# Performance work log

Measured on AMD Instinct MI355X. Metric: run time of the kernel, lower is better.

The kernel has to match this reference:

```python
import jax, jax.numpy as jnp
import numpy as np

N = 50000      # num_nodes
E = 800000     # num_edges (avg degree 16)
D = 128        # input_dim = hidden_dim = output_dim
L = 3          # num_layers
EPS = 1e-5     # BatchNorm eps


def setup_inputs() -> dict:
    key = jax.random.key(0)
    k_x, k_e, k_w, k_b = jax.random.split(key, 4)
    x = jax.random.normal(k_x, (N, D), dtype=jnp.float32)
    edge_index = jax.random.randint(k_e, (2, E), 0, N, dtype=jnp.int32)
    # Stacked per-layer params: GCN weight/bias + BatchNorm gamma/beta
    Ws = jax.random.normal(k_w, (L, D, D), dtype=jnp.float32) * (1.0 / np.sqrt(D))
    bs = jax.random.normal(k_b, (L, D), dtype=jnp.float32) * 0.01
    gammas = jnp.ones((L, D), dtype=jnp.float32)
    betas = jnp.zeros((L, D), dtype=jnp.float32)
    return {"x": x, "edge_index": edge_index, "Ws": Ws, "bs": bs,
            "gammas": gammas, "betas": betas}


def reference(x, edge_index, Ws, bs, gammas, betas):
    """CausalGNN forward: L x (GCNConv -> BN(train stats) -> ReLU[not last]) with residuals.
    Dropout p=0 (deterministic). GCNConv is PyG-style: add self-loops, symmetric
    D^{-1/2} (A+I) D^{-1/2} normalization, linear transform + bias."""
    src, dst = edge_index[0], edge_index[1]
    # degree including self-loop (+1), computed at aggregation index
    deg = jax.ops.segment_sum(jnp.ones((E,), jnp.float32), dst, num_segments=N) + 1.0
    dis = jax.lax.rsqrt(deg)                       # deg >= 1, safe
    norm = dis[src] * dis[dst]                      # [E] edge norm
    self_norm = dis * dis                           # [N] self-loop norm = 1/deg

    for i in range(L):
        h = x @ Ws[i]                               # [N, D]
        # scatter-add aggregation of normalized neighbor messages
        agg = jax.ops.segment_sum(h[src] * norm[:, None], dst, num_segments=N)
        agg = agg + self_norm[:, None] * h + bs[i]
        # BatchNorm1d (training mode: biased batch statistics over nodes)
        mean = jnp.mean(agg, axis=0)
        var = jnp.mean(jnp.square(agg - mean), axis=0)
        y = gammas[i] * (agg - mean) * jax.lax.rsqrt(var + EPS) + betas[i]
        if i < L - 1:
            y = jax.nn.relu(y)
        x = x + y if i > 0 else y                   # residual (dims match)
    return x
```

## Files before the change

kernel.cpp:

```cpp
#include <hip/hip_runtime.h>
#include <hip/hip_bf16.h>
#include <hip/hip_fp16.h>

#define N_ 50000
#define E_ 800000
#define D_ 128
#define L_ 3

#define GG 782
#define NB 391
#define BCAP 3072
#define PB 200
#define PE 4000

typedef _Float16 half8 __attribute__((ext_vector_type(8)));
typedef float f32x4 __attribute__((ext_vector_type(4)));


__device__ inline float4 hcvt(uint2 u) {
    __half2 h0 = *(__half2*)&u.x;
    __half2 h1 = *(__half2*)&u.y;
    float2 f0 = __half22float2(h0);
    float2 f1 = __half22float2(h1);
    return make_float4(f0.x, f0.y, f1.x, f1.y);
}

__device__ inline unsigned pkh(float a, float b) {
    __half2 h = __floats2half2_rn(a, b);
    return *(unsigned*)&h;
}

__device__ inline unsigned short pkh1(float a) {
    _Float16 h = (_Float16)a;
    return *(unsigned short*)&h;
}


__global__ __launch_bounds__(256) void k_part(const int* __restrict__ src,
                                              const int* __restrict__ dst,
                                              const float* __restrict__ Ws,
                                              unsigned short* __restrict__ Wb,
                                              int* __restrict__ bucket_cnt,
                                              unsigned int* __restrict__ binned) {
    int b = blockIdx.x;
    if (b >= PB) {
        int l = b - PB;
        const float* Wl = Ws + l * 16384;
        unsigned short* Wo = Wb + l * 16384;
        for (int i = threadIdx.x; i < 16384; i += 256) {
            int n = i >> 7, k = i & 127;
            Wo[n * 128 + k] = pkh1(Wl[k * 128 + n]);
        }
        return;
    }
    __shared__ int hcnt[NB];
    __shared__ int hbase[NB];
    int t = threadIdx.x;
    for (int i = t; i < NB; i += 256) hcnt[i] = 0;
    __syncthreads();
    int e0 = b * PE;
    int dreg[16], sreg[16], oreg[16];
#pragma unroll
    for (int it = 0; it < 16; ++it) {
        int i = t + it * 256;
        if (i < PE) {
            int e = e0 + i;
            int d = dst[e];
            dreg[it] = d;
            sreg[it] = src[e];
            oreg[it] = atomicAdd(&hcnt[d >> 7], 1);
        }
    }
    __syncthreads();
    for (int i = t; i < NB; i += 256) {
        int c = hcnt[i];
        hbase[i] = c ? atomicAdd(&bucket_cnt[i], c) : 0;
    }
    __syncthreads();
#pragma unroll
    for (int it = 0; it < 16; ++it) {
        int i = t + it * 256;
        if (i < PE) {
            int d = dreg[it];
            int bk = d >> 7;
            binned[bk * BCAP + hbase[bk] + oreg[it]] =
                ((unsigned)(d & 127) << 16) | (unsigned)sreg[it];
        }
    }
}


__global__ __launch_bounds__(512) void k_bscan(const int* __restrict__ bucket_cnt,
                                               int* __restrict__ bucket_base,
                                               int* __restrict__ row_ptr) {
    __shared__ int wsum[8];
    int t = threadIdx.x;
    int lane = t & 63, wid = t >> 6;
    int v = (t < NB) ? bucket_cnt[t] : 0;
    int inc = v;
#pragma unroll
    for (int o = 1; o < 64; o <<= 1) {
        int u = __shfl_up(inc, o);
        if (lane >= o) inc += u;
    }
    if (lane == 63) wsum[wid] = inc;
    __syncthreads();
    if (wid == 0) {
        int w = (lane < 8) ? wsum[lane] : 0;
#pragma unroll
        for (int o = 1; o < 8; o <<= 1) {
            int u = __shfl_up(w, o);
            if (lane >= o) w += u;
        }
        if (lane < 8) wsum[lane] = w;
    }
    __syncthreads();
    int woff = wid ? wsum[wid - 1] : 0;
    if (t < NB) bucket_base[t] = inc + woff - v;
    if (t == 0) row_ptr[N_] = E_;
}


__device__ __forceinline__ void bin_body(const unsigned int* __restrict__ binned,
                                         const int* __restrict__ bucket_cnt,
                                         const int* __restrict__ bucket_base,
                                         int* __restrict__ row_ptr,
                                         float* __restrict__ dis,
                                         int* __restrict__ csr_src, int b) {
    __shared__ int h[128];
    __shared__ int hs[128];
    __shared__ int wtot[2];
    int t = threadIdx.x;
    if (t < 128) h[t] = 0;
    __syncthreads();
    int cnt  = bucket_cnt[b];
    int base = bucket_base[b];
    const unsigned int* bp = binned + b * BCAP;
    unsigned int pk[12];
    int off[12];
#pragma unroll
    for (int it = 0; it < 12; ++it) {
        int i = t + it * 256;
        if (i < cnt) {
            unsigned int p = bp[i];
            pk[it] = p;
            off[it] = atomicAdd(&h[p >> 16], 1);
        }
    }
    __syncthreads();
    int v = (t < 128) ? h[t] : 0;
    int lane = t & 63, wid = t >> 6;
    int inc = v;
#pragma unroll
    for (int o = 1; o < 64; o <<= 1) {
        int u = __shfl_up(inc, o);
        if (lane >= o) inc += u;
    }
    if (lane == 63 && wid < 2) wtot[wid] = inc;
    __syncthreads();
    if (wid == 1) inc += wtot[0];
    if (t < 128) {
        hs[t] = inc - v;
        int node = b * 128 + t;
        if (node < N_) {
            dis[node] = rsqrtf((float)v + 1.0f);
            row_ptr[node] = base + (inc - v);
        }
    }
    __syncthreads();
#pragma unroll
    for (int it = 0; it < 12; ++it) {
        int i = t + it * 256;
        if (i < cnt) {
            unsigned int p = pk[it];
            csr_src[base + hs[p >> 16] + off[it]] = (int)(p & 0xFFFFu);
        }
    }
}


__device__ __forceinline__ void gemm_body(const float* __restrict__ Xin,
                                          const unsigned short* __restrict__ Wb,
                                          uint4* __restrict__ Hb,
                                          const float* __restrict__ st,
                                          const float* __restrict__ gamma,
                                          const float* __restrict__ beta,
                                          const unsigned short* __restrict__ resH,
                                          unsigned short* __restrict__ xoutH,
                                          int blk) {
    __shared__ unsigned short wt[128 * 136];
    __shared__ unsigned short xb[64 * 136];
    __shared__ float sab[256];
    int t  = threadIdx.x;
    int r0 = blk * 64;

    if (st) {
        if (t < 128) {
            float s = 0.f, s2 = 0.f;
#pragma unroll
            for (int k = 0; k < 8; ++k) {
                s  += st[k * 256 + t];
                s2 += st[k * 256 + 128 + t];
            }
            float mean = s * (1.0f / N_);
            float var  = s2 * (1.0f / N_) - mean * mean;
            float a = gamma[t] * rsqrtf(var + 1e-5f);
            sab[t]       = a;
            sab[128 + t] = beta[t] - mean * a;
        }
        __syncthreads();
    }

#pragma unroll
    for (int j = 0; j < 8; ++j) {
        int i = t + 256 * j;
        int row = i >> 4, c16 = i & 15;
        *(uint4*)&wt[row * 136 + c16 * 8] = ((const uint4*)Wb)[i];
    }
#pragma unroll
    for (int j = 0; j < 8; ++j) {
        int g   = t + 256 * j;
        int row = g >> 5;
        int c4  = (g & 31) * 4;
        int gr  = r0 + row;
        float4 v = make_float4(0.f, 0.f, 0.f, 0.f);
        if (gr < N_) {
            v = *(const float4*)(Xin + gr * 128 + c4);
            if (st) {
                v.x = fmaxf(sab[c4] * v.x + sab[128 + c4], 0.f);
                v.y = fmaxf(sab[c4 + 1] * v.y + sab[128 + c4 + 1], 0.f);
                v.z = fmaxf(sab[c4 + 2] * v.z + sab[128 + c4 + 2], 0.f);
                v.w = fmaxf(sab[c4 + 3] * v.w + sab[128 + c4 + 3], 0.f);
                if (resH) {
                    float4 rr = hcvt(*(const uint2*)(resH + gr * 128 + c4));
                    v.x += rr.x; v.y += rr.y; v.z += rr.z; v.w += rr.w;
                }
            }
        }
        uint2 p;
        p.x = pkh(v.x, v.y);
        p.y = pkh(v.z, v.w);
        if (st && gr < N_) *(uint2*)(xoutH + gr * 128 + c4) = p;
        *(uint2*)&xb[row * 136 + c4] = p;
    }
    __syncthreads();

    int wv   = t >> 6;
    int lane = t & 63;
    int ln   = lane & 15;
    int quad = lane >> 4;

    const unsigned short* arow = &xb[(wv * 16 + ln) * 136 + quad * 8];
    half8 af[4];
#pragma unroll
    for (int ks = 0; ks < 4; ++ks) af[ks] = *(const half8*)(arow + ks * 32);

    f32x4 acc[8];
#pragma unroll
    for (int ct = 0; ct < 8; ++ct) acc[ct] = (f32x4){0.f, 0.f, 0.f, 0.f};

#pragma unroll
    for (int ct = 0; ct < 8; ++ct) {
        const unsigned short* wp = &wt[(ct * 16 + ln) * 136 + quad * 8];
#pragma unroll
        for (int ks = 0; ks < 4; ++ks) {
            half8 bf = *(const half8*)(wp + ks * 32);
            acc[ct] = __builtin_amdgcn_mfma_f32_16x16x32_f16(af[ks], bf, acc[ct], 0, 0, 0);
        }
    }

    __syncthreads();
#pragma unroll
    for (int ct = 0; ct < 8; ++ct) {
#pragma unroll
        for (int reg = 0; reg < 4; ++reg) {
            int lrow = wv * 16 + quad * 4 + reg;
            xb[lrow * 136 + ct * 16 + ln] = pkh1(acc[ct][reg]);
        }
    }
    __syncthreads();
#pragma unroll
    for (int j = 0; j < 4; ++j) {
        int i = t + 256 * j;
        int row = i >> 4, c16 = i & 15;
        int gr = r0 + row;
        if (gr < N_) Hb[gr * 16 + c16] = *(uint4*)&xb[row * 136 + c16 * 8];
    }
}


__global__ __launch_bounds__(256) void k_fillg(const unsigned int* __restrict__ binned,
                                               const int* __restrict__ bucket_cnt,
                                               const int* __restrict__ bucket_base,
                                               int* __restrict__ row_ptr,
                                               float* __restrict__ dis,
                                               int* __restrict__ csr_src,
                                               const float* __restrict__ x,
                                               const unsigned short* __restrict__ Wb,
                                               uint4* __restrict__ Hb) {
    int b = blockIdx.x;
    if (b < NB) {
        bin_body(binned, bucket_cnt, bucket_base, row_ptr, dis, csr_src, b);
    } else {
        gemm_body(x, Wb, Hb, nullptr, nullptr, nullptr, nullptr, nullptr, b - NB);
    }
}


__global__ __launch_bounds__(256) void k_gemm(const float* __restrict__ Xin,
                                              const unsigned short* __restrict__ Wb,
                                              uint4* __restrict__ Hb,
                                              const float* __restrict__ st,
                                              const float* __restrict__ gamma,
                                              const float* __restrict__ beta,
                                              const unsigned short* __restrict__ resH,
                                              unsigned short* __restrict__ xoutH) {
    gemm_body(Xin, Wb, Hb, st, gamma, beta, resH, xoutH, blockIdx.x);
}


__global__ __launch_bounds__(256) void k_agg(const uint4* __restrict__ Hb,
                                             const int* __restrict__ row_ptr,
                                             const int* __restrict__ csr_src,
                                             const float* __restrict__ dis,
                                             const float* __restrict__ bias,
                                             float4* __restrict__ AGG,
                                             float* __restrict__ stats2) {
    int tid  = threadIdx.x;
    int sub  = tid >> 4;
    int lane = tid & 15;
    int node = blockIdx.x * 16 + sub;

    int beg = row_ptr[node], end = row_ptr[node + 1];
    float dn = dis[node];
    uint4 su = Hb[node * 16 + lane];
    float4 f0s = hcvt(make_uint2(su.x, su.y));
    float4 f1s = hcvt(make_uint2(su.z, su.w));
    float4 acc0, acc1;
    acc0.x = dn * f0s.x; acc0.y = dn * f0s.y; acc0.z = dn * f0s.z; acc0.w = dn * f0s.w;
    acc1.x = dn * f1s.x; acc1.y = dn * f1s.y; acc1.z = dn * f1s.z; acc1.w = dn * f1s.w;

    for (int c = beg; c < end; c += 16) {
        int m = end - c; if (m > 16) m = 16;
        int idx = 0; float dsv = 0.f;
        if (lane < m) { idx = csr_src[c + lane]; dsv = dis[idx]; }
        int j = 0;
        for (; j + 4 <= m; j += 4) {
            int s0 = __shfl(idx, j, 16);
            int s1 = __shfl(idx, j + 1, 16);
            int s2 = __shfl(idx, j + 2, 16);
            int s3 = __shfl(idx, j + 3, 16);
            float d0 = __shfl(dsv, j, 16);
            float d1 = __shfl(dsv, j + 1, 16);
            float d2 = __shfl(dsv, j + 2, 16);
            float d3 = __shfl(dsv, j + 3, 16);
            uint4 a0 = Hb[s0 * 16 + lane];
            uint4 a1 = Hb[s1 * 16 + lane];
            uint4 a2 = Hb[s2 * 16 + lane];
            uint4 a3 = Hb[s3 * 16 + lane];
            float4 f00 = hcvt(make_uint2(a0.x, a0.y)), f01 = hcvt(make_uint2(a0.z, a0.w));
            float4 f10 = hcvt(make_uint2(a1.x, a1.y)), f11 = hcvt(make_uint2(a1.z, a1.w));
            float4 f20 = hcvt(make_uint2(a2.x, a2.y)), f21 = hcvt(make_uint2(a2.z, a2.w));
            float4 f30 = hcvt(make_uint2(a3.x, a3.y)), f31 = hcvt(make_uint2(a3.z, a3.w));
            acc0.x += d0 * f00.x + d1 * f10.x + d2 * f20.x + d3 * f30.x;
            acc0.y += d0 * f00.y + d1 * f10.y + d2 * f20.y + d3 * f30.y;
            acc0.z += d0 * f00.z + d1 * f10.z + d2 * f20.z + d3 * f30.z;
            acc0.w += d0 * f00.w + d1 * f10.w + d2 * f20.w + d3 * f30.w;
            acc1.x += d0 * f01.x + d1 * f11.x + d2 * f21.x + d3 * f31.x;
            acc1.y += d0 * f01.y + d1 * f11.y + d2 * f21.y + d3 * f31.y;
            acc1.z += d0 * f01.z + d1 * f11.z + d2 * f21.z + d3 * f31.z;
            acc1.w += d0 * f01.w + d1 * f11.w + d2 * f21.w + d3 * f31.w;
        }
        for (; j < m; ++j) {
            int s0 = __shfl(idx, j, 16);
            float d0 = __shfl(dsv, j, 16);
            uint4 a0 = Hb[s0 * 16 + lane];
            float4 f00 = hcvt(make_uint2(a0.x, a0.y)), f01 = hcvt(make_uint2(a0.z, a0.w));
            acc0.x += d0 * f00.x; acc0.y += d0 * f00.y;
            acc0.z += d0 * f00.z; acc0.w += d0 * f00.w;
            acc1.x += d0 * f01.x; acc1.y += d0 * f01.y;
            acc1.z += d0 * f01.z; acc1.w += d0 * f01.w;
        }
    }

    float4 b0 = *(const float4*)(bias + lane * 8);
    float4 b1 = *(const float4*)(bias + lane * 8 + 4);
    float4 r0, r1;
    r0.x = dn * acc0.x + b0.x; r0.y = dn * acc0.y + b0.y;
    r0.z = dn * acc0.z + b0.z; r0.w = dn * acc0.w + b0.w;
    r1.x = dn * acc1.x + b1.x; r1.y = dn * acc1.y + b1.y;
    r1.z = dn * acc1.z + b1.z; r1.w = dn * acc1.w + b1.w;
    AGG[node * 32 + lane * 2]     = r0;
    AGG[node * 32 + lane * 2 + 1] = r1;

    __shared__ float sbuf[16][128];
    float4* sp = (float4*)&sbuf[sub][lane * 8];
    sp[0] = r0; sp[1] = r1;
    __syncthreads();
    if (tid < 128) {
        float s = 0.f, s2 = 0.f;
#pragma unroll
        for (int k = 0; k < 16; ++k) {
            float v = sbuf[k][tid];
            s += v; s2 += v * v;
        }
        float* stp = stats2 + (blockIdx.x & 7) * 256;
        atomicAdd(&stp[tid], s);
        atomicAdd(&stp[128 + tid], s2);
    }
}


__global__ __launch_bounds__(256) void k_normF(const float4* __restrict__ AGG,
                                               const unsigned short* __restrict__ resH,
                                               const float* __restrict__ st,
                                               const float* __restrict__ gamma,
                                               const float* __restrict__ beta,
                                               float4* __restrict__ OUT) {
    __shared__ float sab[256];
    int t = threadIdx.x;
    if (t < 128) {
        float s = 0.f, s2 = 0.f;
#pragma unroll
        for (int k = 0; k < 8; ++k) {
            s  += st[k * 256 + t];
            s2 += st[k * 256 + 128 + t];
        }
        float mean = s * (1.0f / N_);
        float var  = s2 * (1.0f / N_) - mean * mean;
        float a = gamma[t] * rsqrtf(var + 1e-5f);
        sab[t]       = a;
        sab[128 + t] = beta[t] - mean * a;
    }
    __syncthreads();
    for (int i = blockIdx.x * 256 + t; i < N_ * 32; i += gridDim.x * 256) {
        int f4 = (i & 31) * 4;
        float4 v = AGG[i];
        float4 rr = hcvt(((const uint2*)resH)[i]);
        v.x = sab[f4] * v.x + sab[128 + f4] + rr.x;
        v.y = sab[f4 + 1] * v.y + sab[128 + f4 + 1] + rr.y;
        v.z = sab[f4 + 2] * v.z + sab[128 + f4 + 2] + rr.z;
        v.w = sab[f4 + 3] * v.w + sab[128 + f4 + 3] + rr.w;
        OUT[i] = v;
    }
}


extern "C" void kernel_launch(void* const* d_in, const int* in_sizes, int n_in,
                              void* d_out, int out_size, void* d_ws, size_t ws_size,
                              hipStream_t stream) {
    const float* x      = (const float*)d_in[0];
    const int*   ei     = (const int*)d_in[1];
    const float* Ws     = (const float*)d_in[2];
    const float* bs     = (const float*)d_in[3];
    const float* gammas = (const float*)d_in[4];
    const float* betas  = (const float*)d_in[5];
    float* out = (float*)d_out;

    const int* src = ei;
    const int* dst = ei + E_;

    char* w = (char*)d_ws;
    float* stats2      = (float*)(w + 0);
    int*   bucket_cnt  = (int*)(w + 24576);
    int*   bucket_base = (int*)(w + 26144);
    int*   row_ptr     = (int*)(w + 27712);
    float* dis         = (float*)(w + 227728);
    int*   csr_src     = (int*)(w + 427728);
    uint4* Hb          = (uint4*)(w + 3627776);
    unsigned short* XBh = (unsigned short*)(w + 16427776);
    unsigned short* Wb  = (unsigned short*)(w + 29227776);
    float* AGG = out;

    unsigned int* binned = (unsigned int*)XBh;

    hipMemsetAsync(d_ws, 0, 26144, stream);

    k_part<<<PB + 3, 256, 0, stream>>>(src, dst, Ws, Wb, bucket_cnt, binned);
    k_bscan<<<1, 512, 0, stream>>>(bucket_cnt, bucket_base, row_ptr);
    k_fillg<<<NB + GG, 256, 0, stream>>>(binned, bucket_cnt, bucket_base, row_ptr,
                                         dis, csr_src, x, Wb, Hb);

    k_agg<<<N_ / 16, 256, 0, stream>>>(Hb, row_ptr, csr_src, dis, bs,
                                       (float4*)AGG, stats2);
    k_gemm<<<GG, 256, 0, stream>>>(AGG, Wb + 16384, Hb,
                                   stats2, gammas, betas, nullptr, XBh);
    k_agg<<<N_ / 16, 256, 0, stream>>>(Hb, row_ptr, csr_src, dis, bs + D_,
                                       (float4*)AGG, stats2 + 2048);
    k_gemm<<<GG, 256, 0, stream>>>(AGG, Wb + 32768, Hb,
                                   stats2 + 2048, gammas + D_, betas + D_, XBh, XBh);
    k_agg<<<N_ / 16, 256, 0, stream>>>(Hb, row_ptr, csr_src, dis, bs + 2 * D_,
                                       (float4*)AGG, stats2 + 4096);
    k_normF<<<1024, 256, 0, stream>>>((const float4*)AGG, XBh,
                                      stats2 + 4096, gammas + 2 * D_, betas + 2 * D_,
                                      (float4*)out);
}
```

Measured before the change: 263.4 us.

## Prescale GEMM output by dis, store intermediate aggregates in fp16, unroll gather by 8

The GEMM epilogue now multiplies each output row by its dis value, so layers 2 and 3 aggregation skip the per-edge dis lookup and multiply. The first two aggregation outputs are written as fp16 and read back as fp16 by the next GEMM, halving that intermediate traffic. The gather loop also gains an 8-wide unrolled stage to keep more loads in flight. The cost is extra fp16 rounding of the aggregate and of the prescaled features before batch-norm statistics, plus higher register pressure from the wider unroll.

```diff
diff --git a/kernel.cpp b/kernel.cpp
--- a/kernel.cpp
+++ b/kernel.cpp
@@ -179,8 +179,10 @@
 }
 
 
-__device__ __forceinline__ void gemm_body(const float* __restrict__ Xin,
+template <bool IN16>
+__device__ __forceinline__ void gemm_body(const void* __restrict__ Xin,
                                           const unsigned short* __restrict__ Wb,
+                                          const float* __restrict__ disp,
                                           uint4* __restrict__ Hb,
                                           const float* __restrict__ st,
                                           const float* __restrict__ gamma,
@@ -225,7 +227,11 @@
         int gr  = r0 + row;
         float4 v = make_float4(0.f, 0.f, 0.f, 0.f);
         if (gr < N_) {
-            v = *(const float4*)(Xin + gr * 128 + c4);
+            if constexpr (IN16) {
+                v = hcvt(*(const uint2*)((const unsigned short*)Xin + gr * 128 + c4));
+            } else {
+                v = *(const float4*)((const float*)Xin + gr * 128 + c4);
+            }
             if (st) {
                 v.x = fmaxf(sab[c4] * v.x + sab[128 + c4], 0.f);
                 v.y = fmaxf(sab[c4 + 1] * v.y + sab[128 + c4 + 1], 0.f);
@@ -269,13 +275,21 @@
         }
     }
 
+    float dr[4] = {1.f, 1.f, 1.f, 1.f};
+    if (disp) {
+#pragma unroll
+        for (int reg = 0; reg < 4; ++reg) {
+            int r = r0 + wv * 16 + quad * 4 + reg;
+            dr[reg] = disp[r < N_ ? r : (N_ - 1)];
+        }
+    }
     __syncthreads();
 #pragma unroll
     for (int ct = 0; ct < 8; ++ct) {
 #pragma unroll
         for (int reg = 0; reg < 4; ++reg) {
             int lrow = wv * 16 + quad * 4 + reg;
-            xb[lrow * 136 + ct * 16 + ln] = pkh1(acc[ct][reg]);
+            xb[lrow * 136 + ct * 16 + ln] = pkh1(acc[ct][reg] * dr[reg]);
         }
     }
     __syncthreads();
@@ -302,29 +316,32 @@
     if (b < NB) {
         bin_body(binned, bucket_cnt, bucket_base, row_ptr, dis, csr_src, b);
     } else {
-        gemm_body(x, Wb, Hb, nullptr, nullptr, nullptr, nullptr, nullptr, b - NB);
-    }
-}
-
-
-__global__ __launch_bounds__(256) void k_gemm(const float* __restrict__ Xin,
+        gemm_body<false>(x, Wb, nullptr, Hb, nullptr, nullptr, nullptr, nullptr,
+                         nullptr, b - NB);
+    }
+}
+
+
+__global__ __launch_bounds__(256) void k_gemm(const unsigned short* __restrict__ Xin,
                                               const unsigned short* __restrict__ Wb,
+                                              const float* __restrict__ disp,
                                               uint4* __restrict__ Hb,
                                               const float* __restrict__ st,
                                               const float* __restrict__ gamma,
                                               const float* __restrict__ beta,
                                               const unsigned short* __restrict__ resH,
                                               unsigned short* __restrict__ xoutH) {
-    gemm_body(Xin, Wb, Hb, st, gamma, beta, resH, xoutH, blockIdx.x);
-}
-
-
+    gemm_body<true>(Xin, Wb, disp, Hb, st, gamma, beta, resH, xoutH, blockIdx.x);
+}
+
+
+template <bool SCALED, bool OUT16>
 __global__ __launch_bounds__(256) void k_agg(const uint4* __restrict__ Hb,
                                              const int* __restrict__ row_ptr,
                                              const int* __restrict__ csr_src,
                                              const float* __restrict__ dis,
                                              const float* __restrict__ bias,
-                                             float4* __restrict__ AGG,
+                                             void* __restrict__ AGGout,
                                              float* __restrict__ stats2) {
     int tid  = threadIdx.x;
     int sub  = tid >> 4;
@@ -337,49 +354,85 @@
     float4 f0s = hcvt(make_uint2(su.x, su.y));
     float4 f1s = hcvt(make_uint2(su.z, su.w));
     float4 acc0, acc1;
-    acc0.x = dn * f0s.x; acc0.y = dn * f0s.y; acc0.z = dn * f0s.z; acc0.w = dn * f0s.w;
-    acc1.x = dn * f1s.x; acc1.y = dn * f1s.y; acc1.z = dn * f1s.z; acc1.w = dn * f1s.w;
+    if constexpr (SCALED) {
+        acc0 = f0s; acc1 = f1s;
+    } else {
+        acc0.x = dn * f0s.x; acc0.y = dn * f0s.y; acc0.z = dn * f0s.z; acc0.w = dn * f0s.w;
+        acc1.x = dn * f1s.x; acc1.y = dn * f1s.y; acc1.z = dn * f1s.z; acc1.w = dn * f1s.w;
+    }
 
     for (int c = beg; c < end; c += 16) {
         int m = end - c; if (m > 16) m = 16;
         int idx = 0; float dsv = 0.f;
-        if (lane < m) { idx = csr_src[c + lane]; dsv = dis[idx]; }
+        if (lane < m) {
+            idx = csr_src[c + lane];
+            if constexpr (!SCALED) dsv = dis[idx];
+        }
         int j = 0;
+        for (; j + 8 <= m; j += 8) {
+            int s[8]; float d[8]; uint4 a[8];
+#pragma unroll
+            for (int k = 0; k < 8; ++k) {
+                s[k] = __shfl(idx, j + k, 16);
+                if constexpr (!SCALED) d[k] = __shfl(dsv, j + k, 16);
+            }
+#pragma unroll
+            for (int k = 0; k < 8; ++k) a[k] = Hb[s[k] * 16 + lane];
+#pragma unroll
+            for (int k = 0; k < 8; ++k) {
+                float4 f0 = hcvt(make_uint2(a[k].x, a[k].y));
+                float4 f1 = hcvt(make_uint2(a[k].z, a[k].w));
+                if constexpr (SCALED) {
+                    acc0.x += f0.x; acc0.y += f0.y; acc0.z += f0.z; acc0.w += f0.w;
+                    acc1.x += f1.x; acc1.y += f1.y; acc1.z += f1.z; acc1.w += f1.w;
+                } else {
+                    acc0.x += d[k] * f0.x; acc0.y += d[k] * f0.y;
+                    acc0.z += d[k] * f0.z; acc0.w += d[k] * f0.w;
+                    acc1.x += d[k] * f1.x; acc1.y += d[k] * f1.y;
+                    acc1.z += d[k] * f1.z; acc1.w += d[k] * f1.w;
+                }
+            }
+        }
         for (; j + 4 <= m; j += 4) {
-            int s0 = __shfl(idx, j, 16);
-            int s1 = __shfl(idx, j + 1, 16);
-            int s2 = __shfl(idx, j + 2, 16);
-            int s3 = __shfl(idx, j + 3, 16);
-            float d0 = __shfl(dsv, j, 16);
-            float d1 = __shfl(dsv, j + 1, 16);
-            float d2 = __shfl(dsv, j + 2, 16);
-            float d3 = __shfl(dsv, j + 3, 16);
-            uint4 a0 = Hb[s0 * 16 + lane];
-            uint4 a1 = Hb[s1 * 16 + lane];
-            uint4 a2 = Hb[s2 * 16 + lane];
-            uint4 a3 = Hb[s3 * 16 + lane];
-            float4 f00 = hcvt(make_uint2(a0.x, a0.y)), f01 = hcvt(make_uint2(a0.z, a0.w));
-            float4 f10 = hcvt(make_uint2(a1.x, a1.y)), f11 = hcvt(make_uint2(a1.z, a1.w));
-            float4 f20 = hcvt(make_uint2(a2.x, a2.y)), f21 = hcvt(make_uint2(a2.z, a2.w));
-            float4 f30 = hcvt(make_uint2(a3.x, a3.y)), f31 = hcvt(make_uint2(a3.z, a3.w));
-            acc0.x += d0 * f00.x + d1 * f10.x + d2 * f20.x + d3 * f30.x;
-            acc0.y += d0 * f00.y + d1 * f10.y + d2 * f20.y + d3 * f30.y;
-            acc0.z += d0 * f00.z + d1 * f10.z + d2 * f20.z + d3 * f30.z;
-            acc0.w += d0 * f00.w + d1 * f10.w + d2 * f20.w + d3 * f30.w;
-            acc1.x += d0 * f01.x + d1 * f11.x + d2 * f21.x + d3 * f31.x;
-            acc1.y += d0 * f01.y + d1 * f11.y + d2 * f21.y + d3 * f31.y;
-            acc1.z += d0 * f01.z + d1 * f11.z + d2 * f21.z + d3 * f31.z;
-            acc1.w += d0 * f01.w + d1 * f11.w + d2 * f21.w + d3 * f31.w;
+            int s[4]; float d[4]; uint4 a[4];
+#pragma unroll
+            for (int k = 0; k < 4; ++k) {
+                s[k] = __shfl(idx, j + k, 16);
+                if constexpr (!SCALED) d[k] = __shfl(dsv, j + k, 16);
+            }
+#pragma unroll
+            for (int k = 0; k < 4; ++k) a[k] = Hb[s[k] * 16 + lane];
+#pragma unroll
+            for (int k = 0; k < 4; ++k) {
+                float4 f0 = hcvt(make_uint2(a[k].x, a[k].y));
+                float4 f1 = hcvt(make_uint2(a[k].z, a[k].w));
+                if constexpr (SCALED) {
+                    acc0.x += f0.x; acc0.y += f0.y; acc0.z += f0.z; acc0.w += f0.w;
+                    acc1.x += f1.x; acc1.y += f1.y; acc1.z += f1.z; acc1.w += f1.w;
+                } else {
+                    acc0.x += d[k] * f0.x; acc0.y += d[k] * f0.y;
+                    acc0.z += d[k] * f0.z; acc0.w += d[k] * f0.w;
+                    acc1.x += d[k] * f1.x; acc1.y += d[k] * f1.y;
+                    acc1.z += d[k] * f1.z; acc1.w += d[k] * f1.w;
+                }
+            }
         }
         for (; j < m; ++j) {
             int s0 = __shfl(idx, j, 16);
-            float d0 = __shfl(dsv, j, 16);
+            float d0 = 0.f;
+            if constexpr (!SCALED) d0 = __shfl(dsv, j, 16);
             uint4 a0 = Hb[s0 * 16 + lane];
-            float4 f00 = hcvt(make_uint2(a0.x, a0.y)), f01 = hcvt(make_uint2(a0.z, a0.w));
-            acc0.x += d0 * f00.x; acc0.y += d0 * f00.y;
-            acc0.z += d0 * f00.z; acc0.w += d0 * f00.w;
-            acc1.x += d0 * f01.x; acc1.y += d0 * f01.y;
-            acc1.z += d0 * f01.z; acc1.w += d0 * f01.w;
+            float4 f0 = hcvt(make_uint2(a0.x, a0.y));
+            float4 f1 = hcvt(make_uint2(a0.z, a0.w));
+            if constexpr (SCALED) {
+                acc0.x += f0.x; acc0.y += f0.y; acc0.z += f0.z; acc0.w += f0.w;
+                acc1.x += f1.x; acc1.y += f1.y; acc1.z += f1.z; acc1.w += f1.w;
+            } else {
+                acc0.x += d0 * f0.x; acc0.y += d0 * f0.y;
+                acc0.z += d0 * f0.z; acc0.w += d0 * f0.w;
+                acc1.x += d0 * f1.x; acc1.y += d0 * f1.y;
+                acc1.z += d0 * f1.z; acc1.w += d0 * f1.w;
+            }
         }
     }
 
@@ -390,8 +443,16 @@
     r0.z = dn * acc0.z + b0.z; r0.w = dn * acc0.w + b0.w;
     r1.x = dn * acc1.x + b1.x; r1.y = dn * acc1.y + b1.y;
     r1.z = dn * acc1.z + b1.z; r1.w = dn * acc1.w + b1.w;
-    AGG[node * 32 + lane * 2]     = r0;
-    AGG[node * 32 + lane * 2 + 1] = r1;
+
+    if constexpr (OUT16) {
+        uint4 p;
+        p.x = pkh(r0.x, r0.y); p.y = pkh(r0.z, r0.w);
+        p.z = pkh(r1.x, r1.y); p.w = pkh(r1.z, r1.w);
+        ((uint4*)AGGout)[node * 16 + lane] = p;
+    } else {
+        ((float4*)AGGout)[node * 32 + lane * 2]     = r0;
+        ((float4*)AGGout)[node * 32 + lane * 2 + 1] = r1;
+    }
 
     __shared__ float sbuf[16][128];
     float4* sp = (float4*)&sbuf[sub][lane * 8];
@@ -470,6 +531,8 @@
     uint4* Hb          = (uint4*)(w + 3627776);
     unsigned short* XBh = (unsigned short*)(w + 16427776);
     unsigned short* Wb  = (unsigned short*)(w + 29227776);
+
+    unsigned short* AGG16 = (unsigned short*)out;
     float* AGG = out;
 
     unsigned int* binned = (unsigned int*)XBh;
@@ -481,16 +544,16 @@
     k_fillg<<<NB + GG, 256, 0, stream>>>(binned, bucket_cnt, bucket_base, row_ptr,
                                          dis, csr_src, x, Wb, Hb);
 
-    k_agg<<<N_ / 16, 256, 0, stream>>>(Hb, row_ptr, csr_src, dis, bs,
-                                       (float4*)AGG, stats2);
-    k_gemm<<<GG, 256, 0, stream>>>(AGG, Wb + 16384, Hb,
+    k_agg<false, true><<<N_ / 16, 256, 0, stream>>>(Hb, row_ptr, csr_src, dis, bs,
+                                                    AGG16, stats2);
+    k_gemm<<<GG, 256, 0, stream>>>(AGG16, Wb + 16384, dis, Hb,
                                    stats2, gammas, betas, nullptr, XBh);
-    k_agg<<<N_ / 16, 256, 0, stream>>>(Hb, row_ptr, csr_src, dis, bs + D_,
-                                       (float4*)AGG, stats2 + 2048);
-    k_gemm<<<GG, 256, 0, stream>>>(AGG, Wb + 32768, Hb,
+    k_agg<true, true><<<N_ / 16, 256, 0, stream>>>(Hb, row_ptr, csr_src, dis, bs + D_,
+                                                   AGG16, stats2 + 2048);
+    k_gemm<<<GG, 256, 0, stream>>>(AGG16, Wb + 32768, dis, Hb,
                                    stats2 + 2048, gammas + D_, betas + D_, XBh, XBh);
-    k_agg<<<N_ / 16, 256, 0, stream>>>(Hb, row_ptr, csr_src, dis, bs + 2 * D_,
-                                       (float4*)AGG, stats2 + 4096);
+    k_agg<true, false><<<N_ / 16, 256, 0, stream>>>(Hb, row_ptr, csr_src, dis, bs + 2 * D_,
+                                                    AGG, stats2 + 4096);
     k_normF<<<1024, 256, 0, stream>>>((const float4*)AGG, XBh,
                                       stats2 + 4096, gammas + 2 * D_, betas + 2 * D_,
                                       (float4*)out);
```

Result: slower. 268.7 us (+2.0%).

## Prescale GEMM output rows by dis and drop bucket-scan kernel

Applied to the files above, without the earlier changes.

Two changes. The layer-2 and layer-3 GEMMs now multiply each output row by its source-node dis factor before storing H, so the aggregation kernel no longer gathers dis[src] per edge and does plain adds. The separate bucket-scan kernel is removed, and each binning block instead computes its own base offset by summing the counts of all earlier buckets. This saves one launch and a random gather per edge, at the cost of redundant prefix sums in every block and a small change in fp16 rounding of H.

```diff
diff --git a/kernel.cpp b/kernel.cpp
--- a/kernel.cpp
+++ b/kernel.cpp
@@ -90,51 +90,28 @@
 }
 
 
-__global__ __launch_bounds__(512) void k_bscan(const int* __restrict__ bucket_cnt,
-                                               int* __restrict__ bucket_base,
-                                               int* __restrict__ row_ptr) {
-    __shared__ int wsum[8];
-    int t = threadIdx.x;
-    int lane = t & 63, wid = t >> 6;
-    int v = (t < NB) ? bucket_cnt[t] : 0;
-    int inc = v;
-#pragma unroll
-    for (int o = 1; o < 64; o <<= 1) {
-        int u = __shfl_up(inc, o);
-        if (lane >= o) inc += u;
-    }
-    if (lane == 63) wsum[wid] = inc;
-    __syncthreads();
-    if (wid == 0) {
-        int w = (lane < 8) ? wsum[lane] : 0;
-#pragma unroll
-        for (int o = 1; o < 8; o <<= 1) {
-            int u = __shfl_up(w, o);
-            if (lane >= o) w += u;
-        }
-        if (lane < 8) wsum[lane] = w;
-    }
-    __syncthreads();
-    int woff = wid ? wsum[wid - 1] : 0;
-    if (t < NB) bucket_base[t] = inc + woff - v;
-    if (t == 0) row_ptr[N_] = E_;
-}
-
-
 __device__ __forceinline__ void bin_body(const unsigned int* __restrict__ binned,
                                          const int* __restrict__ bucket_cnt,
-                                         const int* __restrict__ bucket_base,
                                          int* __restrict__ row_ptr,
                                          float* __restrict__ dis,
                                          int* __restrict__ csr_src, int b) {
     __shared__ int h[128];
     __shared__ int hs[128];
-    __shared__ int wtot[2];
+    __shared__ int wtot[4];
     int t = threadIdx.x;
+    int lane = t & 63, wid = t >> 6;
+
+    int part = 0;
+    for (int i = t; i < b; i += 256) part += bucket_cnt[i];
+#pragma unroll
+    for (int o = 32; o > 0; o >>= 1) part += __shfl_down(part, o, 64);
+    if (lane == 0) wtot[wid] = part;
     if (t < 128) h[t] = 0;
     __syncthreads();
-    int cnt  = bucket_cnt[b];
-    int base = bucket_base[b];
+    int base = wtot[0] + wtot[1] + wtot[2] + wtot[3];
+    __syncthreads();
+
+    int cnt = bucket_cnt[b];
     const unsigned int* bp = binned + b * BCAP;
     unsigned int pk[12];
     int off[12];
@@ -149,7 +126,6 @@
     }
     __syncthreads();
     int v = (t < 128) ? h[t] : 0;
-    int lane = t & 63, wid = t >> 6;
     int inc = v;
 #pragma unroll
     for (int o = 1; o < 64; o <<= 1) {
@@ -167,6 +143,7 @@
             row_ptr[node] = base + (inc - v);
         }
     }
+    if (b == 0 && t == 0) row_ptr[N_] = E_;
     __syncthreads();
 #pragma unroll
     for (int it = 0; it < 12; ++it) {
@@ -181,6 +158,7 @@
 
 __device__ __forceinline__ void gemm_body(const float* __restrict__ Xin,
                                           const unsigned short* __restrict__ Wb,
+                                          const float* __restrict__ disp,
                                           uint4* __restrict__ Hb,
                                           const float* __restrict__ st,
                                           const float* __restrict__ gamma,
@@ -269,13 +247,21 @@
         }
     }
 
+    float dr[4] = {1.f, 1.f, 1.f, 1.f};
+    if (disp) {
+#pragma unroll
+        for (int reg = 0; reg < 4; ++reg) {
+            int r = r0 + wv * 16 + quad * 4 + reg;
+            dr[reg] = disp[r < N_ ? r : (N_ - 1)];
+        }
+    }
     __syncthreads();
 #pragma unroll
     for (int ct = 0; ct < 8; ++ct) {
 #pragma unroll
         for (int reg = 0; reg < 4; ++reg) {
             int lrow = wv * 16 + quad * 4 + reg;
-            xb[lrow * 136 + ct * 16 + ln] = pkh1(acc[ct][reg]);
+            xb[lrow * 136 + ct * 16 + ln] = pkh1(acc[ct][reg] * dr[reg]);
         }
     }
     __syncthreads();
@@ -291,7 +277,6 @@
 
 __global__ __launch_bounds__(256) void k_fillg(const unsigned int* __restrict__ binned,
                                                const int* __restrict__ bucket_cnt,
-                                               const int* __restrict__ bucket_base,
                                                int* __restrict__ row_ptr,
                                                float* __restrict__ dis,
                                                int* __restrict__ csr_src,
@@ -300,25 +285,28 @@
                                                uint4* __restrict__ Hb) {
     int b = blockIdx.x;
     if (b < NB) {
-        bin_body(binned, bucket_cnt, bucket_base, row_ptr, dis, csr_src, b);
+        bin_body(binned, bucket_cnt, row_ptr, dis, csr_src, b);
     } else {
-        gemm_body(x, Wb, Hb, nullptr, nullptr, nullptr, nullptr, nullptr, b - NB);
+        gemm_body(x, Wb, nullptr, Hb, nullptr, nullptr, nullptr, nullptr,
+                  nullptr, b - NB);
     }
 }
 
 
 __global__ __launch_bounds__(256) void k_gemm(const float* __restrict__ Xin,
                                               const unsigned short* __restrict__ Wb,
+                                              const float* __restrict__ disp,
                                               uint4* __restrict__ Hb,
                                               const float* __restrict__ st,
                                               const float* __restrict__ gamma,
                                               const float* __restrict__ beta,
                                               const unsigned short* __restrict__ resH,
                                               unsigned short* __restrict__ xoutH) {
-    gemm_body(Xin, Wb, Hb, st, gamma, beta, resH, xoutH, blockIdx.x);
-}
-
-
+    gemm_body(Xin, Wb, disp, Hb, st, gamma, beta, resH, xoutH, blockIdx.x);
+}
+
+
+template <bool SCALED>
 __global__ __launch_bounds__(256) void k_agg(const uint4* __restrict__ Hb,
                                              const int* __restrict__ row_ptr,
                                              const int* __restrict__ csr_src,
@@ -337,23 +325,33 @@
     float4 f0s = hcvt(make_uint2(su.x, su.y));
     float4 f1s = hcvt(make_uint2(su.z, su.w));
     float4 acc0, acc1;
-    acc0.x = dn * f0s.x; acc0.y = dn * f0s.y; acc0.z = dn * f0s.z; acc0.w = dn * f0s.w;
-    acc1.x = dn * f1s.x; acc1.y = dn * f1s.y; acc1.z = dn * f1s.z; acc1.w = dn * f1s.w;
+    if constexpr (SCALED) {
+        acc0 = f0s; acc1 = f1s;
+    } else {
+        acc0.x = dn * f0s.x; acc0.y = dn * f0s.y; acc0.z = dn * f0s.z; acc0.w = dn * f0s.w;
+        acc1.x = dn * f1s.x; acc1.y = dn * f1s.y; acc1.z = dn * f1s.z; acc1.w = dn * f1s.w;
+    }
 
     for (int c = beg; c < end; c += 16) {
         int m = end - c; if (m > 16) m = 16;
         int idx = 0; float dsv = 0.f;
-        if (lane < m) { idx = csr_src[c + lane]; dsv = dis[idx]; }
+        if (lane < m) {
+            idx = csr_src[c + lane];
+            if constexpr (!SCALED) dsv = dis[idx];
+        }
         int j = 0;
         for (; j + 4 <= m; j += 4) {
             int s0 = __shfl(idx, j, 16);
             int s1 = __shfl(idx, j + 1, 16);
             int s2 = __shfl(idx, j + 2, 16);
             int s3 = __shfl(idx, j + 3, 16);
-            float d0 = __shfl(dsv, j, 16);
-            float d1 = __shfl(dsv, j + 1, 16);
-            float d2 = __shfl(dsv, j + 2, 16);
-            float d3 = __shfl(dsv, j + 3, 16);
+            float d0 = 1.f, d1 = 1.f, d2 = 1.f, d3 = 1.f;
+            if constexpr (!SCALED) {
+                d0 = __shfl(dsv, j, 16);
+                d1 = __shfl(dsv, j + 1, 16);
+                d2 = __shfl(dsv, j + 2, 16);
+                d3 = __shfl(dsv, j + 3, 16);
+            }
             uint4 a0 = Hb[s0 * 16 + lane];
             uint4 a1 = Hb[s1 * 16 + lane];
             uint4 a2 = Hb[s2 * 16 + lane];
@@ -362,34 +360,52 @@
             float4 f10 = hcvt(make_uint2(a1.x, a1.y)), f11 = hcvt(make_uint2(a1.z, a1.w));
             float4 f20 = hcvt(make_uint2(a2.x, a2.y)), f21 = hcvt(make_uint2(a2.z, a2.w));
             float4 f30 = hcvt(make_uint2(a3.x, a3.y)), f31 = hcvt(make_uint2(a3.z, a3.w));
-            acc0.x += d0 * f00.x + d1 * f10.x + d2 * f20.x + d3 * f30.x;
-            acc0.y += d0 * f00.y + d1 * f10.y + d2 * f20.y + d3 * f30.y;
-            acc0.z += d0 * f00.z + d1 * f10.z + d2 * f20.z + d3 * f30.z;
-            acc0.w += d0 * f00.w + d1 * f10.w + d2 * f20.w + d3 * f30.w;
-            acc1.x += d0 * f01.x + d1 * f11.x + d2 * f21.x + d3 * f31.x;
-            acc1.y += d0 * f01.y + d1 * f11.y + d2 * f21.y + d3 * f31.y;
-            acc1.z += d0 * f01.z + d1 * f11.z + d2 * f21.z + d3 * f31.z;
-            acc1.w += d0 * f01.w + d1 * f11.w + d2 * f21.w + d3 * f31.w;
+            if constexpr (SCALED) {
+                acc0.x += f00.x + f10.x + f20.x + f30.x;
+                acc0.y += f00.y + f10.y + f20.y + f30.y;
+                acc0.z += f00.z + f10.z + f20.z + f30.z;
+                acc0.w += f00.w + f10.w + f20.w + f30.w;
+                acc1.x += f01.x + f11.x + f21.x + f31.x;
+                acc1.y += f01.y + f11.y + f21.y + f31.y;
+                acc1.z += f01.z + f11.z + f21.z + f31.z;
+                acc1.w += f01.w + f11.w + f21.w + f31.w;
+            } else {
+                acc0.x += d0 * f00.x + d1 * f10.x + d2 * f20.x + d3 * f30.x;
+                acc0.y += d0 * f00.y + d1 * f10.y + d2 * f20.y + d3 * f30.y;
+                acc0.z += d0 * f00.z + d1 * f10.z + d2 * f20.z + d3 * f30.z;
+                acc0.w += d0 * f00.w + d1 * f10.w + d2 * f20.w + d3 * f30.w;
+                acc1.x += d0 * f01.x + d1 * f11.x + d2 * f21.x + d3 * f31.x;
+                acc1.y += d0 * f01.y + d1 * f11.y + d2 * f21.y + d3 * f31.y;
+                acc1.z += d0 * f01.z + d1 * f11.z + d2 * f21.z + d3 * f31.z;
+                acc1.w += d0 * f01.w + d1 * f11.w + d2 * f21.w + d3 * f31.w;
+            }
         }
         for (; j < m; ++j) {
             int s0 = __shfl(idx, j, 16);
-            float d0 = __shfl(dsv, j, 16);
+            float d0 = 1.f;
+            if constexpr (!SCALED) d0 = __shfl(dsv, j, 16);
             uint4 a0 = Hb[s0 * 16 + lane];
             float4 f00 = hcvt(make_uint2(a0.x, a0.y)), f01 = hcvt(make_uint2(a0.z, a0.w));
-            acc0.x += d0 * f00.x; acc0.y += d0 * f00.y;
-            acc0.z += d0 * f00.z; acc0.w += d0 * f00.w;
-            acc1.x += d0 * f01.x; acc1.y += d0 * f01.y;
-            acc1.z += d0 * f01.z; acc1.w += d0 * f01.w;
-        }
-    }
-
+            if constexpr (SCALED) {
+                acc0.x += f00.x; acc0.y += f00.y; acc0.z += f00.z; acc0.w += f00.w;
+                acc1.x += f01.x; acc1.y += f01.y; acc1.z += f01.z; acc1.w += f01.w;
+            } else {
+                acc0.x += d0 * f00.x; acc0.y += d0 * f00.y;
+                acc0.z += d0 * f00.z; acc0.w += d0 * f00.w;
+                acc1.x += d0 * f01.x; acc1.y += d0 * f01.y;
+                acc1.z += d0 * f01.z; acc1.w += d0 * f01.w;
+            }
+        }
+    }
+
+    float dnn = dn;
     float4 b0 = *(const float4*)(bias + lane * 8);
     float4 b1 = *(const float4*)(bias + lane * 8 + 4);
     float4 r0, r1;
-    r0.x = dn * acc0.x + b0.x; r0.y = dn * acc0.y + b0.y;
-    r0.z = dn * acc0.z + b0.z; r0.w = dn * acc0.w + b0.w;
-    r1.x = dn * acc1.x + b1.x; r1.y = dn * acc1.y + b1.y;
-    r1.z = dn * acc1.z + b1.z; r1.w = dn * acc1.w + b1.w;
+    r0.x = dnn * acc0.x + b0.x; r0.y = dnn * acc0.y + b0.y;
+    r0.z = dnn * acc0.z + b0.z; r0.w = dnn * acc0.w + b0.w;
+    r1.x = dnn * acc1.x + b1.x; r1.y = dnn * acc1.y + b1.y;
+    r1.z = dnn * acc1.z + b1.z; r1.w = dnn * acc1.w + b1.w;
     AGG[node * 32 + lane * 2]     = r0;
     AGG[node * 32 + lane * 2 + 1] = r1;
 
@@ -463,7 +479,6 @@
     char* w = (char*)d_ws;
     float* stats2      = (float*)(w + 0);
     int*   bucket_cnt  = (int*)(w + 24576);
-    int*   bucket_base = (int*)(w + 26144);
     int*   row_ptr     = (int*)(w + 27712);
     float* dis         = (float*)(w + 227728);
     int*   csr_src     = (int*)(w + 427728);
@@ -477,20 +492,19 @@
     hipMemsetAsync(d_ws, 0, 26144, stream);
 
     k_part<<<PB + 3, 256, 0, stream>>>(src, dst, Ws, Wb, bucket_cnt, binned);
-    k_bscan<<<1, 512, 0, stream>>>(bucket_cnt, bucket_base, row_ptr);
-    k_fillg<<<NB + GG, 256, 0, stream>>>(binned, bucket_cnt, bucket_base, row_ptr,
+    k_fillg<<<NB + GG, 256, 0, stream>>>(binned, bucket_cnt, row_ptr,
                                          dis, csr_src, x, Wb, Hb);
 
-    k_agg<<<N_ / 16, 256, 0, stream>>>(Hb, row_ptr, csr_src, dis, bs,
-                                       (float4*)AGG, stats2);
-    k_gemm<<<GG, 256, 0, stream>>>(AGG, Wb + 16384, Hb,
+    k_agg<false><<<N_ / 16, 256, 0, stream>>>(Hb, row_ptr, csr_src, dis, bs,
+                                              (float4*)AGG, stats2);
+    k_gemm<<<GG, 256, 0, stream>>>(AGG, Wb + 16384, dis, Hb,
                                    stats2, gammas, betas, nullptr, XBh);
-    k_agg<<<N_ / 16, 256, 0, stream>>>(Hb, row_ptr, csr_src, dis, bs + D_,
-                                       (float4*)AGG, stats2 + 2048);
-    k_gemm<<<GG, 256, 0, stream>>>(AGG, Wb + 32768, Hb,
+    k_agg<true><<<N_ / 16, 256, 0, stream>>>(Hb, row_ptr, csr_src, dis, bs + D_,
+                                             (float4*)AGG, stats2 + 2048);
+    k_gemm<<<GG, 256, 0, stream>>>(AGG, Wb + 32768, dis, Hb,
                                    stats2 + 2048, gammas + D_, betas + D_, XBh, XBh);
-    k_agg<<<N_ / 16, 256, 0, stream>>>(Hb, row_ptr, csr_src, dis, bs + 2 * D_,
-                                       (float4*)AGG, stats2 + 4096);
+    k_agg<true><<<N_ / 16, 256, 0, stream>>>(Hb, row_ptr, csr_src, dis, bs + 2 * D_,
+                                             (float4*)AGG, stats2 + 4096);
     k_normF<<<1024, 256, 0, stream>>>((const float4*)AGG, XBh,
                                       stats2 + 4096, gammas + 2 * D_, betas + 2 * D_,
                                       (float4*)out);
```

After: 257.7 us (median of 2 runs). 1.02x faster.
